# Kernel optimization log

Measured on AMD Instinct MI355X. Metric: run time of the kernel, lower is better.

## Reference

```python
import jax, jax.numpy as jnp
import numpy as np

GROUPS = 8
EPS = 1e-5


def group_norm(x, w, b, groups=GROUPS, eps=EPS):
    B, C, H, W = x.shape
    xg = x.reshape(B, groups, C // groups, H, W)
    mean = xg.mean(axis=(2, 3, 4), keepdims=True)
    var = xg.var(axis=(2, 3, 4), keepdims=True)
    xg = (xg - mean) * jax.lax.rsqrt(var + eps)
    x = xg.reshape(B, C, H, W)
    return x * w[None, :, None, None] + b[None, :, None, None]


def setup_inputs() -> dict:
    key = jax.random.key(0)
    ks = jax.random.split(key, 7)
    C = 512
    x = jax.random.normal(ks[0], (16, C, 32, 32), dtype=jnp.float32)
    norm_w = jnp.ones((C,), dtype=jnp.float32)
    norm_b = jnp.zeros((C,), dtype=jnp.float32)
    s = 1.0 / np.sqrt(C)
    qkv_w = jax.random.uniform(ks[1], (3 * C, C), jnp.float32, -s, s)
    qkv_b = jax.random.uniform(ks[2], (3 * C,), jnp.float32, -s, s)
    proj_w = jax.random.uniform(ks[3], (C, C), jnp.float32, -s, s)
    proj_b = jax.random.uniform(ks[4], (C,), jnp.float32, -s, s)
    return {"x": x, "norm_w": norm_w, "norm_b": norm_b, "qkv_w": qkv_w,
            "qkv_b": qkv_b, "proj_w": proj_w, "proj_b": proj_b}


def reference(x, norm_w, norm_b, qkv_w, qkv_b, proj_w, proj_b):
    B, C, H, W = x.shape
    h_in = x
    xn = group_norm(x, norm_w, norm_b)
    # 1x1 conv == per-pixel linear over channels
    qkv = jnp.einsum('oc,bchw->bohw', qkv_w, xn) + qkv_b[None, :, None, None]
    q, k, v = jnp.split(qkv, 3, axis=1)
    q = q.reshape(B, C, H * W)
    k = k.reshape(B, C, H * W)
    v = v.reshape(B, C, H * W)
    attn = jnp.einsum('bci,bcj->bij', q, k) / jnp.sqrt(jnp.asarray(C, x.dtype))
    attn = jax.nn.softmax(attn, axis=-1)
    out = jnp.einsum('bij,bcj->bci', attn, v).reshape(B, C, H, W)
    out = jnp.einsum('oc,bchw->bohw', proj_w, out) + proj_b[None, :, None, None]
    return h_in + out
```

## Files before the change

kernel.cpp:

```cpp
#include <hip/hip_runtime.h>
#include <stdint.h>

typedef __attribute__((ext_vector_type(4))) float f32x4;
typedef __attribute__((ext_vector_type(8))) __bf16 bf16x8;

__device__ __forceinline__ unsigned short f2bf(float f) {
  union { float f; unsigned u; } v; v.f = f;
  unsigned r = v.u + 0x7FFF + ((v.u >> 16) & 1);
  return (unsigned short)(r >> 16);
}

__device__ __forceinline__ void g2l16(const void* g, void* l) {
  __builtin_amdgcn_global_load_lds((const __attribute__((address_space(1))) void*)g,
                                   (__attribute__((address_space(3))) void*)l, 16, 0, 0);
}

__global__ void cvt_weights(const float* __restrict__ a, const float* __restrict__ p,
                            unsigned short* __restrict__ wa, unsigned short* __restrict__ wp) {
  int i = blockIdx.x * 256 + threadIdx.x;
  if (i < 786432) wa[i] = f2bf(a[i]);
  else wp[i - 786432] = f2bf(p[i - 786432]);
}

__global__ void gn_stats(const float* __restrict__ x, float* __restrict__ stats) {
  int bid = blockIdx.x;
  const float4* p = (const float4*)(x + (size_t)bid * 65536);
  float s = 0.f, ss = 0.f;
  for (int i = threadIdx.x; i < 16384; i += 256) {
    float4 v = p[i];
    s += v.x + v.y + v.z + v.w;
    ss += v.x * v.x + v.y * v.y + v.z * v.z + v.w * v.w;
  }
#pragma unroll
  for (int o = 32; o > 0; o >>= 1) {
    s += __shfl_down(s, o, 64);
    ss += __shfl_down(ss, o, 64);
  }
  __shared__ float red[8];
  int w = threadIdx.x >> 6;
  if ((threadIdx.x & 63) == 0) { red[w] = s; red[4 + w] = ss; }
  __syncthreads();
  if (threadIdx.x == 0) {
    s = red[0] + red[1] + red[2] + red[3];
    ss = red[4] + red[5] + red[6] + red[7];
    float mean = s * (1.f / 65536.f);
    float var = ss * (1.f / 65536.f) - mean * mean;
    stats[2 * bid] = mean;
    stats[2 * bid + 1] = rsqrtf(var + 1e-5f);
  }
}

__global__ void gn_norm_t(const float* __restrict__ x, const float* __restrict__ stats,
                          const float* __restrict__ gw, const float* __restrict__ gb,
                          unsigned short* __restrict__ xnT) {
  __shared__ float tile[64][65];
  int bid = blockIdx.x;
  int pt = bid & 15, ct = (bid >> 4) & 7, b = bid >> 7;
  int t = threadIdx.x;
  float mean = stats[2 * (b * 8 + ct)];
  float rstd = stats[2 * (b * 8 + ct) + 1];
  const float* src = x + ((size_t)(b * 512 + ct * 64)) * 1024 + pt * 64;
#pragma unroll
  for (int i = 0; i < 4; i++) {
    int lin = t + i * 256;
    int c = lin >> 4, p4 = lin & 15;
    float4 v = *(const float4*)(src + (size_t)c * 1024 + p4 * 4);
    float g = gw[ct * 64 + c] * rstd;
    float bb = gb[ct * 64 + c] - mean * g;
    tile[c][p4 * 4 + 0] = v.x * g + bb;
    tile[c][p4 * 4 + 1] = v.y * g + bb;
    tile[c][p4 * 4 + 2] = v.z * g + bb;
    tile[c][p4 * 4 + 3] = v.w * g + bb;
  }
  __syncthreads();
  unsigned short* dst = xnT + ((size_t)b * 1024 + pt * 64) * 512 + ct * 64;
#pragma unroll
  for (int i = 0; i < 4; i++) {
    int lin = t + i * 256;
    int p = lin >> 4, cq = lin & 15;
    ushort4 o;
    o.x = f2bf(tile[cq * 4 + 0][p]);
    o.y = f2bf(tile[cq * 4 + 1][p]);
    o.z = f2bf(tile[cq * 4 + 2][p]);
    o.w = f2bf(tile[cq * 4 + 3][p]);
    *(ushort4*)(dst + (size_t)p * 512 + cq * 4) = o;
  }
}

__global__ void softmax_rows(float* __restrict__ S) {
  size_t row = blockIdx.x;
  float* s = S + row * 1024;
  int t = threadIdx.x;
  float4 v = *(const float4*)(s + t * 4);
  const float scale = 0.04419417382415922f;
  float m = fmaxf(fmaxf(v.x, v.y), fmaxf(v.z, v.w));
#pragma unroll
  for (int o = 32; o > 0; o >>= 1) m = fmaxf(m, __shfl_down(m, o, 64));
  __shared__ float red[8];
  int w = t >> 6;
  if ((t & 63) == 0) red[w] = m;
  __syncthreads();
  m = fmaxf(fmaxf(red[0], red[1]), fmaxf(red[2], red[3]));
  float e0 = __expf((v.x - m) * scale);
  float e1 = __expf((v.y - m) * scale);
  float e2 = __expf((v.z - m) * scale);
  float e3 = __expf((v.w - m) * scale);
  float sum = e0 + e1 + e2 + e3;
#pragma unroll
  for (int o = 32; o > 0; o >>= 1) sum += __shfl_down(sum, o, 64);
  if ((t & 63) == 0) red[4 + w] = sum;
  __syncthreads();
  sum = red[4] + red[5] + red[6] + red[7];
  float inv = 1.0f / sum;
  unsigned short* p = (unsigned short*)s;
  ushort4 o4;
  o4.x = f2bf(e0 * inv); o4.y = f2bf(e1 * inv);
  o4.z = f2bf(e2 * inv); o4.w = f2bf(e3 * inv);
  *(ushort4*)(p + t * 4) = o4;
}

template <int EPI, bool OUT_BF16>
__global__ __launch_bounds__(256) void gemm_bt(
    const unsigned short* __restrict__ A, int lda, long long sA,
    const unsigned short* __restrict__ B, int ldb, long long sB,
    void* __restrict__ Cv, int ldc, long long sC,
    const float* __restrict__ bias,
    const float* __restrict__ res, long long sRes,
    int M, int N, int K, int mt, int nt) {
  __shared__ __align__(16) unsigned short As[128 * 32];
  __shared__ __align__(16) unsigned short Bs[128 * 32];
  int bid = blockIdx.x;
  int per = mt * nt;
  int b = bid / per;
  int r = bid % per;
  int mi = r / nt, ni = r % nt;
  int t = threadIdx.x;
  int l = t & 63, w = t >> 6;
  int wm = w >> 1, wn = w & 1;
  int fr = l & 15;
  int fk = (l >> 4) << 3;
  const unsigned short* Ab = A + (size_t)b * sA + (size_t)(mi * 128) * lda;
  const unsigned short* Bb = B + (size_t)b * sB + (size_t)(ni * 128) * ldb;
  int sr = t >> 2, sk = (t & 3) << 3;
  const unsigned short* gA = Ab + (size_t)sr * lda + sk;
  const unsigned short* gB = Bb + (size_t)sr * ldb + sk;
  unsigned short* lA = As + w * 512;
  unsigned short* lB = Bs + w * 512;
  const unsigned short* ra = As + (wm * 64 + fr) * 32 + fk;
  const unsigned short* rb = Bs + (wn * 64 + fr) * 32 + fk;
  f32x4 acc[4][4] = {};
  for (int k0 = 0; k0 < K; k0 += 32) {
    g2l16(gA, lA);
    g2l16(gA + (size_t)64 * lda, lA + 2048);
    g2l16(gB, lB);
    g2l16(gB + (size_t)64 * ldb, lB + 2048);
    gA += 32; gB += 32;
    __syncthreads();
    bf16x8 af[4], bv[4];
#pragma unroll
    for (int i = 0; i < 4; i++) af[i] = *(const bf16x8*)(ra + i * 512);
#pragma unroll
    for (int j = 0; j < 4; j++) bv[j] = *(const bf16x8*)(rb + j * 512);
#pragma unroll
    for (int i = 0; i < 4; i++)
#pragma unroll
      for (int j = 0; j < 4; j++)
        acc[i][j] = __builtin_amdgcn_mfma_f32_16x16x32_bf16(af[i], bv[j], acc[i][j], 0, 0, 0);
    __syncthreads();
  }
  int crow0 = mi * 128 + wm * 64;
  int ccol0 = ni * 128 + wn * 64;
  int lr = (l >> 4) << 2;
  int lc = l & 15;
#pragma unroll
  for (int i = 0; i < 4; i++) {
#pragma unroll
    for (int j = 0; j < 4; j++) {
      int col = ccol0 + j * 16 + lc;
      float bn = (EPI == 1) ? bias[col] : 0.0f;
#pragma unroll
      for (int e = 0; e < 4; e++) {
        int row = crow0 + i * 16 + lr + e;
        float v = acc[i][j][e];
        if (EPI == 1) v += bn;
        if (EPI == 2 || EPI == 3) v += bias[row];
        if (EPI == 3) v += res[(size_t)b * sRes + (size_t)row * ldc + col];
        size_t o = (size_t)b * sC + (size_t)row * ldc + col;
        if (OUT_BF16) ((unsigned short*)Cv)[o] = f2bf(v);
        else ((float*)Cv)[o] = v;
      }
    }
  }
}

extern "C" void kernel_launch(void* const* d_in, const int* in_sizes, int n_in,
                              void* d_out, int out_size, void* d_ws, size_t ws_size,
                              hipStream_t stream) {
  const float* x = (const float*)d_in[0];
  const float* norm_w = (const float*)d_in[1];
  const float* norm_b = (const float*)d_in[2];
  const float* qkv_w = (const float*)d_in[3];
  const float* qkv_b = (const float*)d_in[4];
  const float* proj_w = (const float*)d_in[5];
  const float* proj_b = (const float*)d_in[6];
  float* out = (float*)d_out;
  char* ws = (char*)d_ws;

  size_t off = 0;
  auto alloc = [&](size_t bytes) {
    off = (off + 255) & ~(size_t)255;
    size_t r = off; off += bytes; return r;
  };
  unsigned short* wqkv  = (unsigned short*)(ws + alloc((size_t)1536 * 512 * 2));
  unsigned short* wproj = (unsigned short*)(ws + alloc((size_t)512 * 512 * 2));
  float* stats          = (float*)(ws + alloc(128 * 2 * 4));
  unsigned short* xnT   = (unsigned short*)(ws + alloc((size_t)16 * 1024 * 512 * 2));
  unsigned short* qkT   = (unsigned short*)(ws + alloc((size_t)16 * 1024 * 1024 * 2));
  unsigned short* vbuf  = (unsigned short*)(ws + alloc((size_t)16 * 512 * 1024 * 2));
  float* Sbuf           = (float*)(ws + alloc((size_t)16 * 1024 * 1024 * 4));

  cvt_weights<<<4096, 256, 0, stream>>>(qkv_w, proj_w, wqkv, wproj);
  gn_stats<<<128, 256, 0, stream>>>(x, stats);
  gn_norm_t<<<2048, 256, 0, stream>>>(x, stats, norm_w, norm_b, xnT);

  gemm_bt<1, true><<<1024, 256, 0, stream>>>(
      xnT, 512, 1024LL * 512, wqkv, 512, 0,
      qkT, 1024, 1024LL * 1024, qkv_b, nullptr, 0, 1024, 1024, 512, 8, 8);

  gemm_bt<2, true><<<512, 256, 0, stream>>>(
      wqkv + (size_t)1024 * 512, 512, 0, xnT, 512, 1024LL * 512,
      vbuf, 1024, 512LL * 1024, qkv_b + 1024, nullptr, 0, 512, 1024, 512, 4, 8);

  gemm_bt<0, false><<<1024, 256, 0, stream>>>(
      qkT, 1024, 1024LL * 1024, qkT + 512, 1024, 1024LL * 1024,
      Sbuf, 1024, 1024LL * 1024, nullptr, nullptr, 0, 1024, 1024, 512, 8, 8);

  softmax_rows<<<16384, 256, 0, stream>>>(Sbuf);

  gemm_bt<0, true><<<512, 256, 0, stream>>>(
      (const unsigned short*)Sbuf, 2048, 2048LL * 1024, vbuf, 1024, 512LL * 1024,
      qkT, 512, 1024LL * 512, nullptr, nullptr, 0, 1024, 512, 1024, 8, 4);

  gemm_bt<3, false><<<512, 256, 0, stream>>>(
      wproj, 512, 0, qkT, 512, 1024LL * 512,
      out, 1024, 512LL * 1024, proj_b, x, 512LL * 1024, 512, 1024, 512, 4, 8);
}
```

Before: 293.9 us.

## Fuse attention into a flash-attention kernel and merge group norm passes

```diff
diff --git a/kernel.cpp b/kernel.cpp
--- a/kernel.cpp
+++ b/kernel.cpp
@@ -22,11 +22,18 @@
   else wp[i - 786432] = f2bf(p[i - 786432]);
 }
 
-__global__ void gn_stats(const float* __restrict__ x, float* __restrict__ stats) {
+__global__ __launch_bounds__(256) void gn_fused(
+    const float* __restrict__ x, const float* __restrict__ gw, const float* __restrict__ gb,
+    unsigned short* __restrict__ xnT) {
+  __shared__ float tile[64][65];
+  __shared__ float red[8];
+  __shared__ float mv[2];
   int bid = blockIdx.x;
+  int g = bid & 7, b = bid >> 3;
+  int t = threadIdx.x;
   const float4* p = (const float4*)(x + (size_t)bid * 65536);
   float s = 0.f, ss = 0.f;
-  for (int i = threadIdx.x; i < 16384; i += 256) {
+  for (int i = t; i < 16384; i += 256) {
     float4 v = p[i];
     s += v.x + v.y + v.z + v.w;
     ss += v.x * v.x + v.y * v.y + v.z * v.z + v.w * v.w;
@@ -36,87 +43,47 @@
     s += __shfl_down(s, o, 64);
     ss += __shfl_down(ss, o, 64);
   }
-  __shared__ float red[8];
-  int w = threadIdx.x >> 6;
-  if ((threadIdx.x & 63) == 0) { red[w] = s; red[4 + w] = ss; }
+  int w = t >> 6;
+  if ((t & 63) == 0) { red[w] = s; red[4 + w] = ss; }
   __syncthreads();
-  if (threadIdx.x == 0) {
+  if (t == 0) {
     s = red[0] + red[1] + red[2] + red[3];
     ss = red[4] + red[5] + red[6] + red[7];
     float mean = s * (1.f / 65536.f);
     float var = ss * (1.f / 65536.f) - mean * mean;
-    stats[2 * bid] = mean;
-    stats[2 * bid + 1] = rsqrtf(var + 1e-5f);
-  }
-}
-
-__global__ void gn_norm_t(const float* __restrict__ x, const float* __restrict__ stats,
-                          const float* __restrict__ gw, const float* __restrict__ gb,
-                          unsigned short* __restrict__ xnT) {
-  __shared__ float tile[64][65];
-  int bid = blockIdx.x;
-  int pt = bid & 15, ct = (bid >> 4) & 7, b = bid >> 7;
-  int t = threadIdx.x;
-  float mean = stats[2 * (b * 8 + ct)];
-  float rstd = stats[2 * (b * 8 + ct) + 1];
-  const float* src = x + ((size_t)(b * 512 + ct * 64)) * 1024 + pt * 64;
-#pragma unroll
-  for (int i = 0; i < 4; i++) {
-    int lin = t + i * 256;
-    int c = lin >> 4, p4 = lin & 15;
-    float4 v = *(const float4*)(src + (size_t)c * 1024 + p4 * 4);
-    float g = gw[ct * 64 + c] * rstd;
-    float bb = gb[ct * 64 + c] - mean * g;
-    tile[c][p4 * 4 + 0] = v.x * g + bb;
-    tile[c][p4 * 4 + 1] = v.y * g + bb;
-    tile[c][p4 * 4 + 2] = v.z * g + bb;
-    tile[c][p4 * 4 + 3] = v.w * g + bb;
+    mv[0] = mean; mv[1] = rsqrtf(var + 1e-5f);
   }
   __syncthreads();
-  unsigned short* dst = xnT + ((size_t)b * 1024 + pt * 64) * 512 + ct * 64;
-#pragma unroll
-  for (int i = 0; i < 4; i++) {
-    int lin = t + i * 256;
-    int p = lin >> 4, cq = lin & 15;
-    ushort4 o;
-    o.x = f2bf(tile[cq * 4 + 0][p]);
-    o.y = f2bf(tile[cq * 4 + 1][p]);
-    o.z = f2bf(tile[cq * 4 + 2][p]);
-    o.w = f2bf(tile[cq * 4 + 3][p]);
-    *(ushort4*)(dst + (size_t)p * 512 + cq * 4) = o;
-  }
-}
-
-__global__ void softmax_rows(float* __restrict__ S) {
-  size_t row = blockIdx.x;
-  float* s = S + row * 1024;
-  int t = threadIdx.x;
-  float4 v = *(const float4*)(s + t * 4);
-  const float scale = 0.04419417382415922f;
-  float m = fmaxf(fmaxf(v.x, v.y), fmaxf(v.z, v.w));
-#pragma unroll
-  for (int o = 32; o > 0; o >>= 1) m = fmaxf(m, __shfl_down(m, o, 64));
-  __shared__ float red[8];
-  int w = t >> 6;
-  if ((t & 63) == 0) red[w] = m;
-  __syncthreads();
-  m = fmaxf(fmaxf(red[0], red[1]), fmaxf(red[2], red[3]));
-  float e0 = __expf((v.x - m) * scale);
-  float e1 = __expf((v.y - m) * scale);
-  float e2 = __expf((v.z - m) * scale);
-  float e3 = __expf((v.w - m) * scale);
-  float sum = e0 + e1 + e2 + e3;
-#pragma unroll
-  for (int o = 32; o > 0; o >>= 1) sum += __shfl_down(sum, o, 64);
-  if ((t & 63) == 0) red[4 + w] = sum;
-  __syncthreads();
-  sum = red[4] + red[5] + red[6] + red[7];
-  float inv = 1.0f / sum;
-  unsigned short* p = (unsigned short*)s;
-  ushort4 o4;
-  o4.x = f2bf(e0 * inv); o4.y = f2bf(e1 * inv);
-  o4.z = f2bf(e2 * inv); o4.w = f2bf(e3 * inv);
-  *(ushort4*)(p + t * 4) = o4;
+  float mean = mv[0], rstd = mv[1];
+  const float* src = x + (size_t)bid * 65536;
+  for (int ch = 0; ch < 16; ch++) {
+#pragma unroll
+    for (int i = 0; i < 4; i++) {
+      int lin = t + i * 256;
+      int c = lin >> 4, p4 = lin & 15;
+      float4 v = *(const float4*)(src + (size_t)c * 1024 + ch * 64 + p4 * 4);
+      float gg = gw[g * 64 + c] * rstd;
+      float bb = gb[g * 64 + c] - mean * gg;
+      tile[c][p4 * 4 + 0] = v.x * gg + bb;
+      tile[c][p4 * 4 + 1] = v.y * gg + bb;
+      tile[c][p4 * 4 + 2] = v.z * gg + bb;
+      tile[c][p4 * 4 + 3] = v.w * gg + bb;
+    }
+    __syncthreads();
+    unsigned short* dst = xnT + ((size_t)b * 1024 + ch * 64) * 512 + g * 64;
+#pragma unroll
+    for (int i = 0; i < 4; i++) {
+      int lin = t + i * 256;
+      int pp = lin >> 4, cq = lin & 15;
+      ushort4 o;
+      o.x = f2bf(tile[cq * 4 + 0][pp]);
+      o.y = f2bf(tile[cq * 4 + 1][pp]);
+      o.z = f2bf(tile[cq * 4 + 2][pp]);
+      o.w = f2bf(tile[cq * 4 + 3][pp]);
+      *(ushort4*)(dst + (size_t)pp * 512 + cq * 4) = o;
+    }
+    __syncthreads();
+  }
 }
 
 template <int EPI, bool OUT_BF16>
@@ -193,6 +160,161 @@
   }
 }
 
+__global__ __launch_bounds__(512) void flash_attn(
+    const unsigned short* __restrict__ qkT, const unsigned short* __restrict__ vbuf,
+    unsigned short* __restrict__ obuf) {
+  __shared__ __align__(16) unsigned short Ks[2 * 16 * 64 * 32];
+  __shared__ __align__(16) float Slds[64 * 68];
+  __shared__ __align__(16) unsigned short Plds[2 * 64 * 40];
+  __shared__ float mrow[64], lrow[64], scl[64];
+
+  const float SC = 0.04419417382415922f;
+  int bid = blockIdx.x;
+  int logical = (bid & 7) * 32 + (bid >> 3);
+  int b = logical >> 4, it = logical & 15;
+  int i0 = it * 64;
+  int tid = threadIdx.x;
+  int l = tid & 63, w = tid >> 6;
+  int fr = l & 15, fq = l >> 4;
+  int wm2 = w >> 2;
+  int nf = w & 3;
+  int d0 = w * 64;
+
+  const size_t bq = (size_t)b * 1048576;
+  const size_t bv = (size_t)b * 524288;
+
+  const unsigned short* qr = qkT + bq + (size_t)(i0 + wm2 * 32 + fr) * 1024 + fq * 8;
+  bf16x8 q[2][16];
+#pragma unroll
+  for (int p2 = 0; p2 < 2; p2++)
+#pragma unroll
+    for (int ks = 0; ks < 16; ks++)
+      q[p2][ks] = *(const bf16x8*)(qr + p2 * 16384 + ks * 32);
+
+  int srow = (tid >> 2) & 63;
+  int scc = (tid & 3) * 8;
+  const unsigned short* kg0 = qkT + bq + 512 + (size_t)srow * 1024 + scc;
+  char* ldsK = (char*)Ks;
+
+#pragma unroll
+  for (int call = 0; call < 8; call++) {
+    int panel = call * 2 + (tid >> 8);
+    g2l16(kg0 + (size_t)0 * 65536 + panel * 32, ldsK + call * 8192 + w * 1024);
+  }
+  if (tid < 64) { mrow[tid] = -3e38f; lrow[tid] = 0.f; }
+  __syncthreads();
+
+  f32x4 acc[4][4] = {};
+  const unsigned short* vb = vbuf + bv + (size_t)(d0 + fr) * 1024 + fq * 8;
+
+  for (int jt = 0; jt < 16; jt++) {
+    int cur = jt & 1;
+    if (jt < 15) {
+      const unsigned short* kg = kg0 + (size_t)(jt + 1) * 65536;
+      char* dst = ldsK + (cur ^ 1) * 65536;
+#pragma unroll
+      for (int call = 0; call < 8; call++) {
+        int panel = call * 2 + (tid >> 8);
+        g2l16(kg + panel * 32, dst + call * 8192 + w * 1024);
+      }
+    }
+    {
+      const char* kb = ldsK + cur * 65536 + (nf * 16 + fr) * 64 + fq * 16;
+      f32x4 s0 = {0.f, 0.f, 0.f, 0.f}, s1 = {0.f, 0.f, 0.f, 0.f};
+#pragma unroll
+      for (int ks = 0; ks < 16; ks++) {
+        bf16x8 kf = *(const bf16x8*)(kb + ks * 4096);
+        s0 = __builtin_amdgcn_mfma_f32_16x16x32_bf16(q[0][ks], kf, s0, 0, 0, 0);
+        s1 = __builtin_amdgcn_mfma_f32_16x16x32_bf16(q[1][ks], kf, s1, 0, 0, 0);
+      }
+      int col = nf * 16 + (l & 15);
+      float* sp = Slds + (wm2 * 32 + fq * 4) * 68 + col;
+#pragma unroll
+      for (int e = 0; e < 4; e++) sp[e * 68] = s0[e];
+#pragma unroll
+      for (int e = 0; e < 4; e++) sp[(16 + e) * 68] = s1[e];
+    }
+    __syncthreads();
+
+    {
+      int r = tid >> 3, s8 = tid & 7;
+      const float* srowp = Slds + r * 68 + s8 * 8;
+      float4 a = *(const float4*)srowp;
+      float4 c = *(const float4*)(srowp + 4);
+      float mx = fmaxf(fmaxf(fmaxf(a.x, a.y), fmaxf(a.z, a.w)),
+                       fmaxf(fmaxf(c.x, c.y), fmaxf(c.z, c.w)));
+      mx = fmaxf(mx, __shfl_xor(mx, 1, 64));
+      mx = fmaxf(mx, __shfl_xor(mx, 2, 64));
+      mx = fmaxf(mx, __shfl_xor(mx, 4, 64));
+      float mold = mrow[r];
+      float mnew = fmaxf(mold, mx);
+      float e0 = __expf((a.x - mnew) * SC), e1 = __expf((a.y - mnew) * SC);
+      float e2 = __expf((a.z - mnew) * SC), e3 = __expf((a.w - mnew) * SC);
+      float e4 = __expf((c.x - mnew) * SC), e5 = __expf((c.y - mnew) * SC);
+      float e6 = __expf((c.z - mnew) * SC), e7 = __expf((c.w - mnew) * SC);
+      float sum = e0 + e1 + e2 + e3 + e4 + e5 + e6 + e7;
+      sum += __shfl_xor(sum, 1, 64);
+      sum += __shfl_xor(sum, 2, 64);
+      sum += __shfl_xor(sum, 4, 64);
+      uint4 pw;
+      pw.x = f2bf(e0) | ((unsigned)f2bf(e1) << 16);
+      pw.y = f2bf(e2) | ((unsigned)f2bf(e3) << 16);
+      pw.z = f2bf(e4) | ((unsigned)f2bf(e5) << 16);
+      pw.w = f2bf(e6) | ((unsigned)f2bf(e7) << 16);
+      *(uint4*)((char*)Plds + (s8 >> 2) * 5120 + r * 80 + (s8 & 3) * 16) = pw;
+      if (s8 == 0) {
+        float sf = __expf((mold - mnew) * SC);
+        lrow[r] = lrow[r] * sf + sum;
+        mrow[r] = mnew;
+        scl[r] = sf;
+      }
+    }
+    __syncthreads();
+
+    {
+      f32x4 sc4[4];
+#pragma unroll
+      for (int mi = 0; mi < 4; mi++) sc4[mi] = *(const f32x4*)(scl + mi * 16 + fq * 4);
+#pragma unroll
+      for (int mi = 0; mi < 4; mi++)
+#pragma unroll
+        for (int nj = 0; nj < 4; nj++) acc[mi][nj] *= sc4[mi];
+#pragma unroll
+      for (int kp = 0; kp < 2; kp++) {
+        bf16x8 pf[4];
+#pragma unroll
+        for (int mi = 0; mi < 4; mi++)
+          pf[mi] = *(const bf16x8*)((const char*)Plds + kp * 5120 + (mi * 16 + fr) * 80 + fq * 16);
+#pragma unroll
+        for (int nj = 0; nj < 4; nj++) {
+          bf16x8 vf = *(const bf16x8*)(vb + nj * 16384 + jt * 64 + kp * 32);
+#pragma unroll
+          for (int mi = 0; mi < 4; mi++)
+            acc[mi][nj] = __builtin_amdgcn_mfma_f32_16x16x32_bf16(pf[mi], vf, acc[mi][nj], 0, 0, 0);
+        }
+      }
+    }
+  }
+
+  f32x4 linv[4];
+#pragma unroll
+  for (int mi = 0; mi < 4; mi++) {
+    f32x4 lv = *(const f32x4*)(lrow + mi * 16 + fq * 4);
+#pragma unroll
+    for (int e = 0; e < 4; e++) linv[mi][e] = 1.0f / lv[e];
+  }
+  unsigned short* ob = obuf + bv + (size_t)i0 * 512 + d0 + fr;
+#pragma unroll
+  for (int mi = 0; mi < 4; mi++)
+#pragma unroll
+    for (int nj = 0; nj < 4; nj++)
+#pragma unroll
+      for (int e = 0; e < 4; e++) {
+        int row = mi * 16 + fq * 4 + e;
+        ob[(size_t)row * 512 + nj * 16] = f2bf(acc[mi][nj][e] * linv[mi][e]);
+      }
+}
+
 extern "C" void kernel_launch(void* const* d_in, const int* in_sizes, int n_in,
                               void* d_out, int out_size, void* d_ws, size_t ws_size,
                               hipStream_t stream) {
@@ -213,15 +335,13 @@
   };
   unsigned short* wqkv  = (unsigned short*)(ws + alloc((size_t)1536 * 512 * 2));
   unsigned short* wproj = (unsigned short*)(ws + alloc((size_t)512 * 512 * 2));
-  float* stats          = (float*)(ws + alloc(128 * 2 * 4));
   unsigned short* xnT   = (unsigned short*)(ws + alloc((size_t)16 * 1024 * 512 * 2));
   unsigned short* qkT   = (unsigned short*)(ws + alloc((size_t)16 * 1024 * 1024 * 2));
   unsigned short* vbuf  = (unsigned short*)(ws + alloc((size_t)16 * 512 * 1024 * 2));
-  float* Sbuf           = (float*)(ws + alloc((size_t)16 * 1024 * 1024 * 4));
+  unsigned short* obuf  = (unsigned short*)(ws + alloc((size_t)16 * 1024 * 512 * 2));
 
   cvt_weights<<<4096, 256, 0, stream>>>(qkv_w, proj_w, wqkv, wproj);
-  gn_stats<<<128, 256, 0, stream>>>(x, stats);
-  gn_norm_t<<<2048, 256, 0, stream>>>(x, stats, norm_w, norm_b, xnT);
+  gn_fused<<<128, 256, 0, stream>>>(x, norm_w, norm_b, xnT);
 
   gemm_bt<1, true><<<1024, 256, 0, stream>>>(
       xnT, 512, 1024LL * 512, wqkv, 512, 0,
@@ -231,17 +351,9 @@
       wqkv + (size_t)1024 * 512, 512, 0, xnT, 512, 1024LL * 512,
       vbuf, 1024, 512LL * 1024, qkv_b + 1024, nullptr, 0, 512, 1024, 512, 4, 8);
 
-  gemm_bt<0, false><<<1024, 256, 0, stream>>>(
-      qkT, 1024, 1024LL * 1024, qkT + 512, 1024, 1024LL * 1024,
-      Sbuf, 1024, 1024LL * 1024, nullptr, nullptr, 0, 1024, 1024, 512, 8, 8);
-
-  softmax_rows<<<16384, 256, 0, stream>>>(Sbuf);
-
-  gemm_bt<0, true><<<512, 256, 0, stream>>>(
-      (const unsigned short*)Sbuf, 2048, 2048LL * 1024, vbuf, 1024, 512LL * 1024,
-      qkT, 512, 1024LL * 512, nullptr, nullptr, 0, 1024, 512, 1024, 8, 4);
+  flash_attn<<<256, 512, 0, stream>>>(qkT, vbuf, obuf);
 
   gemm_bt<3, false><<<512, 256, 0, stream>>>(
-      wproj, 512, 0, qkT, 512, 1024LL * 512,
+      wproj, 512, 0, obuf, 512, 1024LL * 512,
       out, 1024, 512LL * 1024, proj_b, x, 512LL * 1024, 512, 1024, 512, 4, 8);
 }
```

Measured after the change: 319.7 us. +8.8%, slower.
